# Performance work log

Measured on AMD Instinct MI355X. Metric: run time of the kernel, lower is better.

## Reference

```python
import jax, jax.numpy as jnp
import numpy as np

B, S, D, H = 2, 2048, 1024, 16
DK = D // H


def setup_inputs() -> dict:
    key = jax.random.key(0)
    ks = jax.random.split(key, 12)
    s = 1.0 / np.sqrt(D)
    inp = {
        "key": jax.random.normal(ks[0], (B, S, D), jnp.float32),
        "query": jax.random.normal(ks[1], (B, S, D), jnp.float32),
        "value": jax.random.normal(ks[2], (B, S, D), jnp.float32),
        # causal mask, broadcastable to (B, H, S, S)
        "mask": jnp.tril(jnp.ones((S, S), jnp.int32))[None, None, :, :],
        "Wq": jax.random.normal(ks[3], (D, D), jnp.float32) * s,
        "bq": jax.random.normal(ks[4], (D,), jnp.float32) * s,
        "Wk": jax.random.normal(ks[5], (D, D), jnp.float32) * s,
        "bk": jax.random.normal(ks[6], (D,), jnp.float32) * s,
        "Wv": jax.random.normal(ks[7], (D, D), jnp.float32) * s,
        "bv": jax.random.normal(ks[8], (D,), jnp.float32) * s,
        "Wo": jax.random.normal(ks[9], (D, D), jnp.float32) * s,
        "bo": jax.random.normal(ks[10], (D,), jnp.float32) * s,
    }
    return inp


def reference(key, query, value, mask, Wq, bq, Wk, bk, Wv, bv, Wo, bo):
    # Linear projections (torch nn.Linear: x @ W.T + b)
    k = key @ Wk.T + bk
    q = query @ Wq.T + bq
    v = value @ Wv.T + bv
    # Faithful to source: raw view (B, H, S, DK), NO transpose --
    # this splits the SEQUENCE dim across heads, matching the original code.
    k = k.reshape(B, H, S, DK)
    q = q.reshape(B, H, S, DK)
    v = v.reshape(B, H, S, DK)
    # Scores scaled by sqrt(d_model) (as in source, not sqrt(d_k))
    scores = jnp.einsum('bhqd,bhkd->bhqk', q, k) / jnp.sqrt(jnp.float32(D))
    scores = jnp.where(mask == 0, -jnp.inf, scores)
    attn = jax.nn.softmax(scores, axis=-1)  # dropout p=0.0 -> identity
    x = jnp.einsum('bhqk,bhkd->bhqd', attn, v)
    # Faithful raw view merge: (B, H, S, DK) -> (B, S, H*DK)
    x = x.reshape(B, S, H * DK)
    return x @ Wo.T + bo
```

## Files before the change

kernel.cpp:

```cpp
#include <hip/hip_runtime.h>
#include <stdint.h>

typedef unsigned short u16;
typedef __attribute__((ext_vector_type(8))) short bfrag8;
typedef __attribute__((ext_vector_type(4))) float f32x4;
typedef __attribute__((ext_vector_type(8))) unsigned short u16x8;
typedef __attribute__((ext_vector_type(4))) unsigned short u16x4;

__device__ __forceinline__ u16 f2bf(float f) {
  union { float f; uint32_t u; } v; v.f = f;
  return (u16)((v.u + 0x7FFFu + ((v.u >> 16) & 1u)) >> 16);
}

__device__ __forceinline__ void gload16(const void* g, void* l) {
  __builtin_amdgcn_global_load_lds(
      (const __attribute__((address_space(1))) void*)g,
      (__attribute__((address_space(3))) void*)l, 16, 0, 0);
}

struct CvtJob { const float* src; u16* dst; int n4; };
struct CvtBatch { CvtJob j[7]; };

__global__ void cvt_batch(CvtBatch b) {
  CvtJob jb = b.j[blockIdx.y];
  int i = blockIdx.x * blockDim.x + threadIdx.x;
  if (i >= jb.n4) return;
  float4 v = reinterpret_cast<const float4*>(jb.src)[i];
  u16x4 o;
  o[0] = f2bf(v.x); o[1] = f2bf(v.y); o[2] = f2bf(v.z); o[3] = f2bf(v.w);
  reinterpret_cast<u16x4*>(jb.dst)[i] = o;
}

struct Gemm3 {
  const u16* A[3];
  const u16* W[3];
  const float* bias[3];
  void* C[3];
};

template<int OUT_F32>
__global__ __launch_bounds__(256, 2) void gemm_nt_bias(Gemm3 g) {
  constexpr int K = 1024, N = 1024;
  constexpr int BK = 32, LDT = BK + 8;
  __shared__ u16 As[128 * LDT];
  __shared__ u16 Bs[128 * LDT];
  const int z = blockIdx.z;
  const u16* __restrict__ A = g.A[z];
  const u16* __restrict__ W = g.W[z];
  const float* __restrict__ bias = g.bias[z];
  const int tid = threadIdx.x;
  const int lane = tid & 63;
  const int lr = lane & 15, lg = lane >> 4;
  const int wave = tid >> 6;
  const int wr = (wave >> 1) * 64, wc = (wave & 1) * 64;
  const int bm = blockIdx.x * 128, bn = blockIdx.y * 128;

  f32x4 acc[4][4] = {};

  for (int k0 = 0; k0 < K; k0 += BK) {
#pragma unroll
    for (int i = 0; i < 2; i++) {
      int u = tid + 256 * i;
      int row = u >> 2, kg = (u & 3) * 8;
      *(u16x8*)&As[row * LDT + kg] = *(const u16x8*)(A + (size_t)(bm + row) * K + k0 + kg);
      *(u16x8*)&Bs[row * LDT + kg] = *(const u16x8*)(W + (size_t)(bn + row) * K + k0 + kg);
    }
    __syncthreads();
    bfrag8 af[4], bf[4];
#pragma unroll
    for (int mi = 0; mi < 4; mi++)
      af[mi] = *(const bfrag8*)&As[(wr + mi * 16 + lr) * LDT + lg * 8];
#pragma unroll
    for (int ni = 0; ni < 4; ni++)
      bf[ni] = *(const bfrag8*)&Bs[(wc + ni * 16 + lr) * LDT + lg * 8];
#pragma unroll
    for (int mi = 0; mi < 4; mi++)
#pragma unroll
      for (int ni = 0; ni < 4; ni++)
        acc[mi][ni] = __builtin_amdgcn_mfma_f32_16x16x32_bf16(af[mi], bf[ni], acc[mi][ni], 0, 0, 0);
    __syncthreads();
  }

  const int col0 = bn + wc + lr;
#pragma unroll
  for (int ni = 0; ni < 4; ni++) {
    int col = col0 + ni * 16;
    float bv = bias[col];
#pragma unroll
    for (int mi = 0; mi < 4; mi++) {
      int row = bm + wr + mi * 16 + lg * 4;
#pragma unroll
      for (int r = 0; r < 4; r++) {
        float v = acc[mi][ni][r] + bv;
        if (OUT_F32)
          ((float*)g.C[z])[(size_t)(row + r) * N + col] = v;
        else
          ((u16*)g.C[z])[(size_t)(row + r) * N + col] = f2bf(v);
      }
    }
  }
}

__global__ void vtrans_kernel(const u16* __restrict__ Vp, u16* __restrict__ VT,
                              unsigned* __restrict__ ctr) {
  if (blockIdx.x == 0 && blockIdx.y == 0 && threadIdx.x < 8) ctr[threadIdx.x * 16] = 0u;
  __shared__ u16 T[64][66];
  const int kt = blockIdx.x, bh = blockIdx.y;
  const int tid = threadIdx.x;
  const u16* src = Vp + (size_t)bh * 131072 + (size_t)kt * 64 * 64;
#pragma unroll
  for (int i = 0; i < 2; i++) {
    int u = tid + 256 * i;
    int row = u >> 3, c = (u & 7) * 8;
    u16x8 v = *(const u16x8*)(src + row * 64 + c);
#pragma unroll
    for (int j = 0; j < 8; j++) T[c + j][row] = v[j];
  }
  __syncthreads();
  u16* dst = VT + (size_t)bh * 131072 + (size_t)kt * 64;
#pragma unroll
  for (int i = 0; i < 2; i++) {
    int u = tid + 256 * i;
    int d = u >> 3, c = (u & 7) * 8;
    u16x8 o = *(const u16x8*)&T[d][c];
    *(u16x8*)(dst + (size_t)d * 2048 + c) = o;
  }
}

__global__ __launch_bounds__(256, 3) void attn_kernel(
    const u16* __restrict__ Qp, const u16* __restrict__ Kp,
    const u16* __restrict__ VT, u16* __restrict__ X,
    unsigned* __restrict__ ctr)
{
  __shared__ __align__(16) u16 Ks[2][64][64];
  __shared__ __align__(16) u16 Vs[2][64][64];
  constexpr int LDP = 72;
  __shared__ __align__(16) u16 Ps[4][16][LDP];
  __shared__ unsigned s_unit;

  const int tid = threadIdx.x, lane = tid & 63, w = tid >> 6;
  const int lr = lane & 15, lg = lane >> 4;
  const int grp = (int)(blockIdx.x & 7);
  unsigned* __restrict__ gctr = ctr + grp * 16;
  const int srow = lane >> 3;
  const int schunk = (lane & 7) ^ srow;
  const float SCALE = 0.03125f;

  for (;;) {
    __syncthreads();
    if (tid == 0) s_unit = atomicAdd(gctr, 1u);
    __syncthreads();
    const unsigned u = s_unit;
    if (u >= 128u) return;
    const int j = 31 - (int)(u >> 2);
    const int bh = grp * 4 + (int)(u & 3u);
    const size_t base = (size_t)bh * 131072;
    const u16* __restrict__ Qb = Qp + base;
    const u16* __restrict__ Kb = Kp + base;
    const u16* __restrict__ Vtb = VT + base;
    const int qrow0 = j * 64 + w * 16;
    const int q = qrow0 + lr;

    bfrag8 qf[2];
#pragma unroll
    for (int ds = 0; ds < 2; ds++)
      qf[ds] = *(const bfrag8*)(Qb + (size_t)(qrow0 + lr) * 64 + ds * 32 + lg * 8);

    f32x4 oacc[4] = {};
    float m_run = -INFINITY, l_run = 0.f;

    auto STAGE = [&](int kt, int bufi) {
      const u16* gk = Kb + (size_t)(kt * 64 + w * 16 + srow) * 64 + schunk * 8;
      gload16(gk,       &Ks[bufi][w * 16][0]);
      gload16(gk + 512, &Ks[bufi][w * 16 + 8][0]);
      const u16* gv = Vtb + (size_t)(w * 16 + srow) * 2048 + kt * 64 + schunk * 8;
      gload16(gv,            &Vs[bufi][w * 16][0]);
      gload16(gv + 8 * 2048, &Vs[bufi][w * 16 + 8][0]);
    };

    STAGE(0, 0);
    __syncthreads();
    int buf = 0;

    for (int kt = 0; kt <= j; kt++) {
      if (kt < j) STAGE(kt + 1, buf ^ 1);

      f32x4 sacc[4];
#pragma unroll
      for (int kf = 0; kf < 4; kf++) sacc[kf] = (f32x4){0.f, 0.f, 0.f, 0.f};
#pragma unroll
      for (int kf = 0; kf < 4; kf++) {
        const int krow = kf * 16 + lr;
        bfrag8 kb0 = *(const bfrag8*)&Ks[buf][krow][((lg) ^ (krow & 7)) * 8];
        bfrag8 kb1 = *(const bfrag8*)&Ks[buf][krow][((lg + 4) ^ (krow & 7)) * 8];
        sacc[kf] = __builtin_amdgcn_mfma_f32_16x16x32_bf16(kb0, qf[0], sacc[kf], 0, 0, 0);
        sacc[kf] = __builtin_amdgcn_mfma_f32_16x16x32_bf16(kb1, qf[1], sacc[kf], 0, 0, 0);
      }

      if (kt == j) {
#pragma unroll
        for (int kf = 0; kf < 4; kf++)
#pragma unroll
          for (int r = 0; r < 4; r++) {
            int kg = kt * 64 + kf * 16 + lg * 4 + r;
            if (kg > q) sacc[kf][r] = -INFINITY;
          }
      }

      float mx01, mx23, smax;
      {
        f32x4 m2 = (f32x4){fmaxf(sacc[0][0], sacc[0][1]), fmaxf(sacc[0][2], sacc[0][3]),
                           fmaxf(sacc[1][0], sacc[1][1]), fmaxf(sacc[1][2], sacc[1][3])};
        f32x4 m3 = (f32x4){fmaxf(sacc[2][0], sacc[2][1]), fmaxf(sacc[2][2], sacc[2][3]),
                           fmaxf(sacc[3][0], sacc[3][1]), fmaxf(sacc[3][2], sacc[3][3])};
        mx01 = fmaxf(fmaxf(m2[0], m2[1]), fmaxf(m2[2], m2[3]));
        mx23 = fmaxf(fmaxf(m3[0], m3[1]), fmaxf(m3[2], m3[3]));
        smax = fmaxf(mx01, mx23);
      }
      smax = fmaxf(smax, __shfl_xor(smax, 16));
      smax = fmaxf(smax, __shfl_xor(smax, 32));

      float mnew = fmaxf(m_run, smax * SCALE);
      float corr = __expf(m_run - mnew);
      m_run = mnew;
#pragma unroll
      for (int df = 0; df < 4; df++)
#pragma unroll
        for (int r = 0; r < 4; r++) oacc[df][r] *= corr;

      float rs = 0.f;
#pragma unroll
      for (int kf = 0; kf < 4; kf++) {
        float p0 = __expf(__builtin_fmaf(sacc[kf][0], SCALE, -mnew));
        float p1 = __expf(__builtin_fmaf(sacc[kf][1], SCALE, -mnew));
        float p2 = __expf(__builtin_fmaf(sacc[kf][2], SCALE, -mnew));
        float p3 = __expf(__builtin_fmaf(sacc[kf][3], SCALE, -mnew));
        rs += (p0 + p1) + (p2 + p3);
        Ps[w][lr][kf * 16 + lg * 4 + 0] = f2bf(p0);
        Ps[w][lr][kf * 16 + lg * 4 + 1] = f2bf(p1);
        Ps[w][lr][kf * 16 + lg * 4 + 2] = f2bf(p2);
        Ps[w][lr][kf * 16 + lg * 4 + 3] = f2bf(p3);
      }
      rs += __shfl_xor(rs, 16);
      rs += __shfl_xor(rs, 32);
      l_run = l_run * corr + rs;

#pragma unroll
      for (int ks = 0; ks < 2; ks++) {
        bfrag8 pa = *(const bfrag8*)&Ps[w][lr][ks * 32 + lg * 8];
#pragma unroll
        for (int df = 0; df < 4; df++) {
          const int vrow = df * 16 + lr;
          bfrag8 vf = *(const bfrag8*)&Vs[buf][vrow][((ks * 4 + lg) ^ (vrow & 7)) * 8];
          oacc[df] = __builtin_amdgcn_mfma_f32_16x16x32_bf16(vf, pa, oacc[df], 0, 0, 0);
        }
      }

      __syncthreads();
      buf ^= 1;
    }

    float inv = 1.0f / l_run;
#pragma unroll
    for (int df = 0; df < 4; df++)
#pragma unroll
      for (int r = 0; r < 4; r++)
        X[base + (size_t)q * 64 + df * 16 + lg * 4 + r] = f2bf(oacc[df][r] * inv);
  }
}

extern "C" void kernel_launch(void* const* d_in, const int* in_sizes, int n_in,
                              void* d_out, int out_size, void* d_ws, size_t ws_size,
                              hipStream_t stream) {
  const float* key   = (const float*)d_in[0];
  const float* query = (const float*)d_in[1];
  const float* value = (const float*)d_in[2];
  const float* Wq = (const float*)d_in[4];
  const float* bq = (const float*)d_in[5];
  const float* Wk = (const float*)d_in[6];
  const float* bk = (const float*)d_in[7];
  const float* Wv = (const float*)d_in[8];
  const float* bv = (const float*)d_in[9];
  const float* Wo = (const float*)d_in[10];
  const float* bo = (const float*)d_in[11];

  u16* ws = (u16*)d_ws;
  const size_t MD = 4096ull * 1024ull;
  u16* qb  = ws;
  u16* kb  = ws + MD;
  u16* vbf = ws + 2 * MD;
  u16* Qp  = ws + 3 * MD;
  u16* Kp  = ws + 4 * MD;
  u16* Vp  = ws + 5 * MD;
  u16* Xb  = ws + 6 * MD;
  u16* wqb = ws + 7 * MD;
  u16* wkb = wqb + 1024 * 1024;
  u16* wvb = wkb + 1024 * 1024;
  u16* wob = wvb + 1024 * 1024;

  CvtBatch cb;
  cb.j[0] = { query, qb, 1048576 };
  cb.j[1] = { key,   kb, 1048576 };
  cb.j[2] = { value, vbf, 1048576 };
  cb.j[3] = { Wq, wqb, 262144 };
  cb.j[4] = { Wk, wkb, 262144 };
  cb.j[5] = { Wv, wvb, 262144 };
  cb.j[6] = { Wo, wob, 262144 };
  cvt_batch<<<dim3(4096, 7), 256, 0, stream>>>(cb);

  Gemm3 g1;
  g1.A[0] = qb;  g1.A[1] = kb;  g1.A[2] = vbf;
  g1.W[0] = wqb; g1.W[1] = wkb; g1.W[2] = wvb;
  g1.bias[0] = bq; g1.bias[1] = bk; g1.bias[2] = bv;
  g1.C[0] = Qp; g1.C[1] = Kp; g1.C[2] = Vp;
  gemm_nt_bias<0><<<dim3(32, 8, 3), 256, 0, stream>>>(g1);

  u16* VT = vbf;
  unsigned* ctr = (unsigned*)qb;
  vtrans_kernel<<<dim3(32, 32), 256, 0, stream>>>(Vp, VT, ctr);

  attn_kernel<<<768, 256, 0, stream>>>(Qp, Kp, VT, Xb, ctr);

  Gemm3 g2;
  g2.A[0] = Xb; g2.W[0] = wob; g2.bias[0] = bo; g2.C[0] = d_out;
  g2.A[1] = g2.A[2] = nullptr; g2.W[1] = g2.W[2] = nullptr;
  g2.bias[1] = g2.bias[2] = nullptr; g2.C[1] = g2.C[2] = nullptr;
  gemm_nt_bias<1><<<dim3(32, 8, 1), 256, 0, stream>>>(g2);
}
```

Measured before the change: 130.1 us.

## Double per-warp query rows to 32, add lazy rescale, exp2, packed bf16 stores

The attention kernel now gives each work unit 128 query rows, so each wave handles two 16-row MFMA tiles and shares each K/V fragment read across both, which halves the LDS K/V traffic per query row. Softmax switches to exp2 with a folded log2e scale and skips the running-max rescale unless the new max exceeds the old one by a threshold. P is written with packed v_cvt_pk_bf16 stores and output rows with vector stores. The costs are higher register pressure, fewer work units (64 instead of 128, which may hurt load balance), and waves whose rows are fully masked idling on trailing K tiles.

Result: slower. 140.6 us (+8.1%).

```diff
diff --git a/kernel.cpp b/kernel.cpp
--- a/kernel.cpp
+++ b/kernel.cpp
@@ -10,6 +10,12 @@
 __device__ __forceinline__ u16 f2bf(float f) {
   union { float f; uint32_t u; } v; v.f = f;
   return (u16)((v.u + 0x7FFFu + ((v.u >> 16) & 1u)) >> 16);
+}
+
+__device__ __forceinline__ uint32_t cvtpk_bf16(float a, float b) {
+  uint32_t r;
+  asm("v_cvt_pk_bf16_f32 %0, %1, %2" : "=v"(r) : "v"(a), "v"(b));
+  return r;
 }
 
 __device__ __forceinline__ void gload16(const void* g, void* l) {
@@ -135,7 +141,7 @@
   __shared__ __align__(16) u16 Ks[2][64][64];
   __shared__ __align__(16) u16 Vs[2][64][64];
   constexpr int LDP = 72;
-  __shared__ __align__(16) u16 Ps[4][16][LDP];
+  __shared__ __align__(16) u16 Ps[4][32][LDP];
   __shared__ unsigned s_unit;
 
   const int tid = threadIdx.x, lane = tid & 63, w = tid >> 6;
@@ -144,30 +150,33 @@
   unsigned* __restrict__ gctr = ctr + grp * 16;
   const int srow = lane >> 3;
   const int schunk = (lane & 7) ^ srow;
-  const float SCALE = 0.03125f;
+  const float C2 = 0.045084939f;
+  const float THR = 11.5f;
 
   for (;;) {
     __syncthreads();
     if (tid == 0) s_unit = atomicAdd(gctr, 1u);
     __syncthreads();
     const unsigned u = s_unit;
-    if (u >= 128u) return;
-    const int j = 31 - (int)(u >> 2);
+    if (u >= 64u) return;
+    const int j = 15 - (int)(u >> 2);
     const int bh = grp * 4 + (int)(u & 3u);
     const size_t base = (size_t)bh * 131072;
     const u16* __restrict__ Qb = Qp + base;
     const u16* __restrict__ Kb = Kp + base;
     const u16* __restrict__ Vtb = VT + base;
-    const int qrow0 = j * 64 + w * 16;
-    const int q = qrow0 + lr;
-
-    bfrag8 qf[2];
-#pragma unroll
-    for (int ds = 0; ds < 2; ds++)
-      qf[ds] = *(const bfrag8*)(Qb + (size_t)(qrow0 + lr) * 64 + ds * 32 + lg * 8);
-
-    f32x4 oacc[4] = {};
-    float m_run = -INFINITY, l_run = 0.f;
+    const int qrow0 = j * 128 + w * 32;
+
+    bfrag8 qf[2][2];
+#pragma unroll
+    for (int mi = 0; mi < 2; mi++)
+#pragma unroll
+      for (int ds = 0; ds < 2; ds++)
+        qf[mi][ds] = *(const bfrag8*)(Qb + (size_t)(qrow0 + mi * 16 + lr) * 64 + ds * 32 + lg * 8);
+
+    f32x4 oacc[2][4] = {};
+    float m_run[2] = {-INFINITY, -INFINITY};
+    float l_run[2] = {0.f, 0.f};
 
     auto STAGE = [&](int kt, int bufi) {
       const u16* gk = Kb + (size_t)(kt * 64 + w * 16 + srow) * 64 + schunk * 8;
@@ -178,81 +187,95 @@
       gload16(gv + 8 * 2048, &Vs[bufi][w * 16 + 8][0]);
     };
 
+    const int ktmax = 2 * j + 1;
+    const int w_ktmax = (qrow0 + 31) >> 6;
+
     STAGE(0, 0);
     __syncthreads();
     int buf = 0;
 
-    for (int kt = 0; kt <= j; kt++) {
-      if (kt < j) STAGE(kt + 1, buf ^ 1);
-
-      f32x4 sacc[4];
-#pragma unroll
-      for (int kf = 0; kf < 4; kf++) sacc[kf] = (f32x4){0.f, 0.f, 0.f, 0.f};
-#pragma unroll
-      for (int kf = 0; kf < 4; kf++) {
-        const int krow = kf * 16 + lr;
-        bfrag8 kb0 = *(const bfrag8*)&Ks[buf][krow][((lg) ^ (krow & 7)) * 8];
-        bfrag8 kb1 = *(const bfrag8*)&Ks[buf][krow][((lg + 4) ^ (krow & 7)) * 8];
-        sacc[kf] = __builtin_amdgcn_mfma_f32_16x16x32_bf16(kb0, qf[0], sacc[kf], 0, 0, 0);
-        sacc[kf] = __builtin_amdgcn_mfma_f32_16x16x32_bf16(kb1, qf[1], sacc[kf], 0, 0, 0);
-      }
-
-      if (kt == j) {
-#pragma unroll
-        for (int kf = 0; kf < 4; kf++)
-#pragma unroll
-          for (int r = 0; r < 4; r++) {
-            int kg = kt * 64 + kf * 16 + lg * 4 + r;
-            if (kg > q) sacc[kf][r] = -INFINITY;
-          }
-      }
-
-      float mx01, mx23, smax;
-      {
-        f32x4 m2 = (f32x4){fmaxf(sacc[0][0], sacc[0][1]), fmaxf(sacc[0][2], sacc[0][3]),
-                           fmaxf(sacc[1][0], sacc[1][1]), fmaxf(sacc[1][2], sacc[1][3])};
-        f32x4 m3 = (f32x4){fmaxf(sacc[2][0], sacc[2][1]), fmaxf(sacc[2][2], sacc[2][3]),
-                           fmaxf(sacc[3][0], sacc[3][1]), fmaxf(sacc[3][2], sacc[3][3])};
-        mx01 = fmaxf(fmaxf(m2[0], m2[1]), fmaxf(m2[2], m2[3]));
-        mx23 = fmaxf(fmaxf(m3[0], m3[1]), fmaxf(m3[2], m3[3]));
-        smax = fmaxf(mx01, mx23);
-      }
-      smax = fmaxf(smax, __shfl_xor(smax, 16));
-      smax = fmaxf(smax, __shfl_xor(smax, 32));
-
-      float mnew = fmaxf(m_run, smax * SCALE);
-      float corr = __expf(m_run - mnew);
-      m_run = mnew;
-#pragma unroll
-      for (int df = 0; df < 4; df++)
-#pragma unroll
-        for (int r = 0; r < 4; r++) oacc[df][r] *= corr;
-
-      float rs = 0.f;
-#pragma unroll
-      for (int kf = 0; kf < 4; kf++) {
-        float p0 = __expf(__builtin_fmaf(sacc[kf][0], SCALE, -mnew));
-        float p1 = __expf(__builtin_fmaf(sacc[kf][1], SCALE, -mnew));
-        float p2 = __expf(__builtin_fmaf(sacc[kf][2], SCALE, -mnew));
-        float p3 = __expf(__builtin_fmaf(sacc[kf][3], SCALE, -mnew));
-        rs += (p0 + p1) + (p2 + p3);
-        Ps[w][lr][kf * 16 + lg * 4 + 0] = f2bf(p0);
-        Ps[w][lr][kf * 16 + lg * 4 + 1] = f2bf(p1);
-        Ps[w][lr][kf * 16 + lg * 4 + 2] = f2bf(p2);
-        Ps[w][lr][kf * 16 + lg * 4 + 3] = f2bf(p3);
-      }
-      rs += __shfl_xor(rs, 16);
-      rs += __shfl_xor(rs, 32);
-      l_run = l_run * corr + rs;
-
-#pragma unroll
-      for (int ks = 0; ks < 2; ks++) {
-        bfrag8 pa = *(const bfrag8*)&Ps[w][lr][ks * 32 + lg * 8];
-#pragma unroll
-        for (int df = 0; df < 4; df++) {
-          const int vrow = df * 16 + lr;
-          bfrag8 vf = *(const bfrag8*)&Vs[buf][vrow][((ks * 4 + lg) ^ (vrow & 7)) * 8];
-          oacc[df] = __builtin_amdgcn_mfma_f32_16x16x32_bf16(vf, pa, oacc[df], 0, 0, 0);
+    for (int kt = 0; kt <= ktmax; kt++) {
+      if (kt < ktmax) STAGE(kt + 1, buf ^ 1);
+
+      if (kt <= w_ktmax) {
+        f32x4 sacc[2][4] = {};
+#pragma unroll
+        for (int kf = 0; kf < 4; kf++) {
+          const int krow = kf * 16 + lr;
+          bfrag8 kb0 = *(const bfrag8*)&Ks[buf][krow][((lg) ^ (krow & 7)) * 8];
+          bfrag8 kb1 = *(const bfrag8*)&Ks[buf][krow][((lg + 4) ^ (krow & 7)) * 8];
+#pragma unroll
+          for (int mi = 0; mi < 2; mi++) {
+            sacc[mi][kf] = __builtin_amdgcn_mfma_f32_16x16x32_bf16(kb0, qf[mi][0], sacc[mi][kf], 0, 0, 0);
+            sacc[mi][kf] = __builtin_amdgcn_mfma_f32_16x16x32_bf16(kb1, qf[mi][1], sacc[mi][kf], 0, 0, 0);
+          }
+        }
+
+        if (kt * 64 + 63 > qrow0) {
+#pragma unroll
+          for (int mi = 0; mi < 2; mi++) {
+            const int q = qrow0 + mi * 16 + lr;
+#pragma unroll
+            for (int kf = 0; kf < 4; kf++)
+#pragma unroll
+              for (int r = 0; r < 4; r++) {
+                int kg = kt * 64 + kf * 16 + lg * 4 + r;
+                if (kg > q) sacc[mi][kf][r] = -INFINITY;
+              }
+          }
+        }
+
+#pragma unroll
+        for (int mi = 0; mi < 2; mi++) {
+          float a0 = fmaxf(fmaxf(sacc[mi][0][0], sacc[mi][0][1]), fmaxf(sacc[mi][0][2], sacc[mi][0][3]));
+          float a1 = fmaxf(fmaxf(sacc[mi][1][0], sacc[mi][1][1]), fmaxf(sacc[mi][1][2], sacc[mi][1][3]));
+          float a2 = fmaxf(fmaxf(sacc[mi][2][0], sacc[mi][2][1]), fmaxf(sacc[mi][2][2], sacc[mi][2][3]));
+          float a3 = fmaxf(fmaxf(sacc[mi][3][0], sacc[mi][3][1]), fmaxf(sacc[mi][3][2], sacc[mi][3][3]));
+          float smax = fmaxf(fmaxf(a0, a1), fmaxf(a2, a3));
+          smax = fmaxf(smax, __shfl_xor(smax, 16));
+          smax = fmaxf(smax, __shfl_xor(smax, 32));
+          float pmax = smax * C2;
+          float mr = m_run[mi];
+          float mnew = mr;
+          if (!__all(pmax <= mr + THR)) {
+            mnew = fmaxf(mr, pmax);
+            float corr = __builtin_amdgcn_exp2f(mr - mnew);
+            l_run[mi] *= corr;
+#pragma unroll
+            for (int df = 0; df < 4; df++)
+#pragma unroll
+              for (int r = 0; r < 4; r++) oacc[mi][df][r] *= corr;
+            m_run[mi] = mnew;
+          }
+          float rs = 0.f;
+#pragma unroll
+          for (int kf = 0; kf < 4; kf++) {
+            float p0 = __builtin_amdgcn_exp2f(__builtin_fmaf(sacc[mi][kf][0], C2, -mnew));
+            float p1 = __builtin_amdgcn_exp2f(__builtin_fmaf(sacc[mi][kf][1], C2, -mnew));
+            float p2 = __builtin_amdgcn_exp2f(__builtin_fmaf(sacc[mi][kf][2], C2, -mnew));
+            float p3 = __builtin_amdgcn_exp2f(__builtin_fmaf(sacc[mi][kf][3], C2, -mnew));
+            rs += (p0 + p1) + (p2 + p3);
+            uint2 pk;
+            pk.x = cvtpk_bf16(p0, p1);
+            pk.y = cvtpk_bf16(p2, p3);
+            *(uint2*)&Ps[w][mi * 16 + lr][kf * 16 + lg * 4] = pk;
+          }
+          rs += __shfl_xor(rs, 16);
+          rs += __shfl_xor(rs, 32);
+          l_run[mi] += rs;
+        }
+
+#pragma unroll
+        for (int ks = 0; ks < 2; ks++) {
+          bfrag8 pa0 = *(const bfrag8*)&Ps[w][lr][ks * 32 + lg * 8];
+          bfrag8 pa1 = *(const bfrag8*)&Ps[w][16 + lr][ks * 32 + lg * 8];
+#pragma unroll
+          for (int df = 0; df < 4; df++) {
+            const int vrow = df * 16 + lr;
+            bfrag8 vf = *(const bfrag8*)&Vs[buf][vrow][((ks * 4 + lg) ^ (vrow & 7)) * 8];
+            oacc[0][df] = __builtin_amdgcn_mfma_f32_16x16x32_bf16(vf, pa0, oacc[0][df], 0, 0, 0);
+            oacc[1][df] = __builtin_amdgcn_mfma_f32_16x16x32_bf16(vf, pa1, oacc[1][df], 0, 0, 0);
+          }
         }
       }
 
@@ -260,12 +283,18 @@
       buf ^= 1;
     }
 
-    float inv = 1.0f / l_run;
-#pragma unroll
-    for (int df = 0; df < 4; df++)
-#pragma unroll
-      for (int r = 0; r < 4; r++)
-        X[base + (size_t)q * 64 + df * 16 + lg * 4 + r] = f2bf(oacc[df][r] * inv);
+#pragma unroll
+    for (int mi = 0; mi < 2; mi++) {
+      float inv = 1.0f / l_run[mi];
+      const int q = qrow0 + mi * 16 + lr;
+#pragma unroll
+      for (int df = 0; df < 4; df++) {
+        u16x4 o;
+#pragma unroll
+        for (int r = 0; r < 4; r++) o[r] = f2bf(oacc[mi][df][r] * inv);
+        *(u16x4*)&X[base + (size_t)q * 64 + df * 16 + lg * 4] = o;
+      }
+    }
   }
 }
 
```
